# Kernel optimization log

Measured on AMD Instinct MI355X. Metric: run time of the kernel, lower is better.

The kernel has to match this reference:

```python
import jax, jax.numpy as jnp
import numpy as np


def _butter1(Wn, highpass):
    """First-order Butterworth digital coefficients (bilinear transform),
    matching scipy.signal.butter(1, Wn, btype). Wn is nyquist-normalized."""
    K = jnp.tan(jnp.pi * Wn / 2.0)
    a1 = (K - 1.0) / (K + 1.0)
    if highpass:
        b0 = 1.0 / (K + 1.0)
        b1 = -b0
    else:
        b0 = K / (K + 1.0)
        b1 = b0
    return b0, b1, a1


def setup_inputs() -> dict:
    key = jax.random.key(0)
    B, T = 128, 262144
    x = jax.random.normal(key, (B, T), dtype=jnp.float32)
    return {
        "x": x,
        "center_freq": jnp.float32(1000.0),  # nn.Parameter
        "bandwidth": jnp.float32(500.0),     # nn.Parameter
        "gain": jnp.float32(1.0),            # nn.Parameter
        "sample_rate": 48000,
    }


def reference(x, center_freq, bandwidth, gain, sample_rate):
    nyq = sample_rate / 2.0
    low_wn = (center_freq - bandwidth / 2.0) / nyq
    high_wn = (center_freq + bandwidth / 2.0) / nyq
    # cascaded 1st-order highpass(low_wn) then lowpass(high_wn) = bandpass
    bh0, bh1, ah1 = _butter1(low_wn, highpass=True)
    bl0, bl1, al1 = _butter1(high_wn, highpass=False)

    xt = x.T  # [T, B] -- scan over time, vectorized over batch
    zeros = jnp.zeros((x.shape[0],), dtype=x.dtype)

    def step(carry, x_t):
        x_prev, y1_prev, y2_prev = carry
        y1 = bh0 * x_t + bh1 * x_prev - ah1 * y1_prev   # highpass stage
        y2 = bl0 * y1 + bl1 * y1_prev - al1 * y2_prev   # lowpass stage
        return (x_t, y1, y2), y2

    _, yt = jax.lax.scan(step, (zeros, zeros, zeros), xt)
    return yt.T * gain  # [B, T]
```

## Files before the change

### kernel.cpp

```cpp
#include <hip/hip_runtime.h>
#include <math.h>

#define B_    128
#define T_    262144
#define L_    16
#define NT_   256
#define WCH_  16
#define OT_   (NT_ * L_)
#define TPR_  (T_ / OT_)
#define NW_   (NT_ / 64)
#define STR_  (L_ + 1)
#define GPB_  4
#define NBLK_ ((B_ * TPR_) / GPB_)

typedef float f32x4 __attribute__((ext_vector_type(4)));

struct Coef {
    float bh0, bh1;
    float p, q, r;
    float blc0, blc1;
};

__device__ inline void iir_step(const Coef& c, float xt, float& x_prev,
                                float& y1, float& y2) {
    float c1 = fmaf(c.bh0,  xt, c.bh1  * x_prev);
    float cx = fmaf(c.blc0, xt, c.blc1 * x_prev);
    float ny1 = fmaf(c.p, y1, c1);
    float ny2 = fmaf(c.q, y1, fmaf(c.r, y2, cx));
    y1 = ny1; y2 = ny2; x_prev = xt;
}

struct Mat { float p, q, r; };
__device__ inline Mat mat_sq(Mat m) {
    Mat o; o.p = m.p * m.p; o.q = m.q * (m.p + m.r); o.r = m.r * m.r; return o;
}
__device__ inline Mat mat_mul(Mat a, Mat b) {
    Mat o; o.p = a.p * b.p; o.q = fmaf(a.q, b.p, a.r * b.q); o.r = a.r * b.r;
    return o;
}
__device__ inline float2 mat_apply_add(Mat m, float2 v, float2 add) {
    float2 o;
    o.x = fmaf(m.p, v.x, add.x);
    o.y = fmaf(m.q, v.x, fmaf(m.r, v.y, add.y));
    return o;
}

__global__ __launch_bounds__(NT_, 4) void bp_kernel(
        const float* __restrict__ x, float* __restrict__ out,
        const float* __restrict__ cfp, const float* __restrict__ bwp,
        const float* __restrict__ gp, const int* __restrict__ srp) {
    __shared__ float  ys[NT_ * STR_];
    __shared__ float2 wagg[WCH_];
    __shared__ float2 wsagg[NW_];

    const int blk  = blockIdx.x;
    const int t    = threadIdx.x;
    const int lane = t & 63;
    const int wav  = t >> 6;

    const int tid0 = blk * GPB_;
    const int row  = tid0 >> 6;
    const int ti0  = tid0 & (TPR_ - 1);
    const long base0 = (long)row * T_ + (long)ti0 * OT_;

    {
        const float* xb = x + base0;
        (void)xb;
    }
    const float* xb0 = x + base0;
    const f32x4* xg0 = (const f32x4*)(xb0 + t * L_);
    f32x4 v0 = __builtin_nontemporal_load(xg0 + 0);
    f32x4 v1 = __builtin_nontemporal_load(xg0 + 1);
    f32x4 v2 = __builtin_nontemporal_load(xg0 + 2);
    f32x4 v3 = __builtin_nontemporal_load(xg0 + 3);
    f32x4 w0 = (f32x4)(0.f), w1 = w0, w2 = w0, w3 = w0;
    if (t < WCH_ && ti0 != 0) {
        const f32x4* wg = (const f32x4*)(xb0 - WCH_ * L_ + t * L_);
        w0 = wg[0]; w1 = wg[1]; w2 = wg[2]; w3 = wg[3];
    }
    float lxp = 0.f;
    if (lane == 0 && (ti0 != 0 || t != 0)) lxp = xb0[t * L_ - 1];

    Coef cf;
    {
        const float PIH = 1.57079632679489661923f;
        float cfv = *cfp, bwv = *bwp;
        float nyq = 0.5f * (float)(*srp);
        float K1 = tanf(PIH * (cfv - 0.5f * bwv) / nyq);
        float K2 = tanf(PIH * (cfv + 0.5f * bwv) / nyq);
        float inv1 = 1.0f / (K1 + 1.0f);
        float ah1 = (K1 - 1.0f) * inv1;
        float inv2 = 1.0f / (K2 + 1.0f);
        float bl0 = K2 * inv2;
        float al1 = (K2 - 1.0f) * inv2;
        cf.bh0 = inv1;
        cf.bh1 = -inv1;
        cf.p = -ah1;
        cf.q = bl0 - bl0 * ah1;
        cf.r = -al1;
        cf.blc0 = bl0 * inv1;
        cf.blc1 = -bl0 * inv1;
    }
    const float gain = *gp;

    Mat A  = { cf.p, cf.q, cf.r };
    Mat AL = A;
    #pragma unroll
    for (int k = 0; k < 4; ++k) AL = mat_sq(AL);
    Mat R = { 1.f, 0.f, 1.f };
    {
        Mat Mp = AL;
        unsigned b = (unsigned)lane;
        #pragma unroll
        for (int k = 0; k < 6; ++k) {
            if (b & 1u) R = mat_mul(Mp, R);
            b >>= 1u;
            if (k < 5) Mp = mat_sq(Mp);
        }
    }

    float2 Scar = make_float2(0.f, 0.f);

    #pragma unroll
    for (int g = 0; g < GPB_; ++g) {
        const long base = base0 + (long)g * OT_;

        float xp = __shfl_up(v3.w, 1u, 64);
        if (lane == 0) xp = lxp;

        float xa[L_];
        xa[0]=v0.x; xa[1]=v0.y; xa[2]=v0.z; xa[3]=v0.w;
        xa[4]=v1.x; xa[5]=v1.y; xa[6]=v1.z; xa[7]=v1.w;
        xa[8]=v2.x; xa[9]=v2.y; xa[10]=v2.z; xa[11]=v2.w;
        xa[12]=v3.x; xa[13]=v3.y; xa[14]=v3.z; xa[15]=v3.w;
        float y2l[L_];
        float y1 = 0.f, y2 = 0.f;
        {
            float xprev = xp;
            #pragma unroll
            for (int i = 0; i < L_; ++i) {
                iir_step(cf, xa[i], xprev, y1, y2);
                y2l[i] = y2;
            }
        }

        if (g == 0) {
            float wxp = __shfl_up(w3.w, 1u, 64);
            if (t < WCH_) {
                float wa[L_];
                wa[0]=w0.x; wa[1]=w0.y; wa[2]=w0.z; wa[3]=w0.w;
                wa[4]=w1.x; wa[5]=w1.y; wa[6]=w1.z; wa[7]=w1.w;
                wa[8]=w2.x; wa[9]=w2.y; wa[10]=w2.z; wa[11]=w2.w;
                wa[12]=w3.x; wa[13]=w3.y; wa[14]=w3.z; wa[15]=w3.w;
                float wy1 = 0.f, wy2 = 0.f;
                float wp = (t == 0) ? 0.f : wxp;
                #pragma unroll
                for (int i = 0; i < L_; ++i) iir_step(cf, wa[i], wp, wy1, wy2);
                wagg[t] = make_float2(wy1, wy2);
            }
        }

        if (g + 1 < GPB_) {
            const float* nxb = x + base + OT_;
            const f32x4* nxg = (const f32x4*)(nxb + t * L_);
            v0 = __builtin_nontemporal_load(nxg + 0);
            v1 = __builtin_nontemporal_load(nxg + 1);
            v2 = __builtin_nontemporal_load(nxg + 2);
            v3 = __builtin_nontemporal_load(nxg + 3);
            if (lane == 0) lxp = nxb[t * L_ - 1];
        }

        float2 a = make_float2(y1, y2);
        Mat Pw = AL;
        #pragma unroll
        for (int o = 1; o < 64; o <<= 1) {
            float vx = __shfl_up(a.x, (unsigned)o, 64);
            float vy = __shfl_up(a.y, (unsigned)o, 64);
            if (lane >= o) {
                a.y = fmaf(Pw.q, vx, fmaf(Pw.r, vy, a.y));
                a.x = fmaf(Pw.p, vx, a.x);
            }
            Pw = mat_sq(Pw);
        }
        float2 ex;
        ex.x = __shfl_up(a.x, 1u, 64);
        ex.y = __shfl_up(a.y, 1u, 64);
        if (lane == 0) { ex.x = 0.f; ex.y = 0.f; }
        if (lane == 63) wsagg[wav] = a;
        __syncthreads();

        float2 S;
        if (g == 0) {
            S = make_float2(0.f, 0.f);
            #pragma unroll
            for (int j = 0; j < WCH_; ++j) S = mat_apply_add(AL, S, wagg[j]);
        } else {
            S = Scar;
        }

        {
            float2 Stot = wsagg[0];
            #pragma unroll
            for (int u = 1; u < NW_; ++u) Stot = mat_apply_add(Pw, Stot, wsagg[u]);
            Mat P2 = mat_sq(Pw);
            Mat P4 = mat_sq(P2);
            Scar = mat_apply_add(P4, S, Stot);
        }

        float2 Sw = S;
        #pragma unroll
        for (int u = 0; u < NW_ - 1; ++u)
            if (wav > u) Sw = mat_apply_add(Pw, Sw, wsagg[u]);
        float2 E = mat_apply_add(R, Sw, ex);

        {
            float c1 = E.x, c2 = E.y;
            float* cp = ys + t * STR_;
            #pragma unroll
            for (int i = 0; i < L_; ++i) {
                float nc1 = cf.p * c1;
                float nc2 = fmaf(cf.q, c1, cf.r * c2);
                c1 = nc1; c2 = nc2;
                cp[i] = (y2l[i] + c2) * gain;
            }
        }
        __syncthreads();

        f32x4* og = (f32x4*)(out + base);
        #pragma unroll
        for (int k = 0; k < 4; ++k) {
            int F = t + NT_ * k;
            int chunk = F >> 2, pos = 4 * (F & 3);
            const float* p = ys + chunk * STR_ + pos;
            f32x4 o; o.x = p[0]; o.y = p[1]; o.z = p[2]; o.w = p[3];
            __builtin_nontemporal_store(o, og + F);
        }
    }
}

extern "C" void kernel_launch(void* const* d_in, const int* in_sizes, int n_in,
                              void* d_out, int out_size, void* d_ws, size_t ws_size,
                              hipStream_t stream) {
    const float* x   = (const float*)d_in[0];
    const float* cfp = (const float*)d_in[1];
    const float* bwp = (const float*)d_in[2];
    const float* gp  = (const float*)d_in[3];
    const int*   srp = (const int*)d_in[4];
    float* out = (float*)d_out;

    dim3 blk(NT_), grd(NBLK_);
    bp_kernel<<<grd, blk, 0, stream>>>(x, out, cfp, bwp, gp, srp);
}
```

Measured before the change: 243.1 us.

## Recompute IIR from carry and store directly, dropping LDS transpose staging

The output pass no longer keeps 16 partial outputs and transposes them through shared memory. Each thread instead reruns the IIR over its 16 inputs starting from the exact carry state and writes four float4 values straight to global memory. This removes one __syncthreads and the LDS round trip per group, and the wave-sum buffer is double-buffered so the next group does not overwrite it early. Groups per block grow from 4 to 8 and the group loop is no longer unrolled. The cost is that each thread now writes a 64-byte span of its own, which is less coalesced than the old transposed stores, and the recurrence arithmetic is doubled.

```diff
diff --git a/kernel.cpp b/kernel.cpp
--- a/kernel.cpp
+++ b/kernel.cpp
@@ -9,8 +9,7 @@
 #define OT_   (NT_ * L_)
 #define TPR_  (T_ / OT_)
 #define NW_   (NT_ / 64)
-#define STR_  (L_ + 1)
-#define GPB_  4
+#define GPB_  8
 #define NBLK_ ((B_ * TPR_) / GPB_)
 
 typedef float f32x4 __attribute__((ext_vector_type(4)));
@@ -49,9 +48,8 @@
         const float* __restrict__ x, float* __restrict__ out,
         const float* __restrict__ cfp, const float* __restrict__ bwp,
         const float* __restrict__ gp, const int* __restrict__ srp) {
-    __shared__ float  ys[NT_ * STR_];
     __shared__ float2 wagg[WCH_];
-    __shared__ float2 wsagg[NW_];
+    __shared__ float2 wsagg[2][NW_];
 
     const int blk  = blockIdx.x;
     const int t    = threadIdx.x;
@@ -63,10 +61,6 @@
     const int ti0  = tid0 & (TPR_ - 1);
     const long base0 = (long)row * T_ + (long)ti0 * OT_;
 
-    {
-        const float* xb = x + base0;
-        (void)xb;
-    }
     const float* xb0 = x + base0;
     const f32x4* xg0 = (const f32x4*)(xb0 + t * L_);
     f32x4 v0 = __builtin_nontemporal_load(xg0 + 0);
@@ -119,55 +113,54 @@
         }
     }
 
+    {
+        float wxp = __shfl_up(w3.w, 1u, 64);
+        if (t < WCH_) {
+            float wy1 = 0.f, wy2 = 0.f;
+            float wp = (t == 0) ? 0.f : wxp;
+            iir_step(cf, w0.x, wp, wy1, wy2); iir_step(cf, w0.y, wp, wy1, wy2);
+            iir_step(cf, w0.z, wp, wy1, wy2); iir_step(cf, w0.w, wp, wy1, wy2);
+            iir_step(cf, w1.x, wp, wy1, wy2); iir_step(cf, w1.y, wp, wy1, wy2);
+            iir_step(cf, w1.z, wp, wy1, wy2); iir_step(cf, w1.w, wp, wy1, wy2);
+            iir_step(cf, w2.x, wp, wy1, wy2); iir_step(cf, w2.y, wp, wy1, wy2);
+            iir_step(cf, w2.z, wp, wy1, wy2); iir_step(cf, w2.w, wp, wy1, wy2);
+            iir_step(cf, w3.x, wp, wy1, wy2); iir_step(cf, w3.y, wp, wy1, wy2);
+            iir_step(cf, w3.z, wp, wy1, wy2); iir_step(cf, w3.w, wp, wy1, wy2);
+            wagg[t] = make_float2(wy1, wy2);
+        }
+    }
+
     float2 Scar = make_float2(0.f, 0.f);
 
-    #pragma unroll
     for (int g = 0; g < GPB_; ++g) {
         const long base = base0 + (long)g * OT_;
 
         float xp = __shfl_up(v3.w, 1u, 64);
         if (lane == 0) xp = lxp;
 
-        float xa[L_];
-        xa[0]=v0.x; xa[1]=v0.y; xa[2]=v0.z; xa[3]=v0.w;
-        xa[4]=v1.x; xa[5]=v1.y; xa[6]=v1.z; xa[7]=v1.w;
-        xa[8]=v2.x; xa[9]=v2.y; xa[10]=v2.z; xa[11]=v2.w;
-        xa[12]=v3.x; xa[13]=v3.y; xa[14]=v3.z; xa[15]=v3.w;
-        float y2l[L_];
         float y1 = 0.f, y2 = 0.f;
         {
             float xprev = xp;
-            #pragma unroll
-            for (int i = 0; i < L_; ++i) {
-                iir_step(cf, xa[i], xprev, y1, y2);
-                y2l[i] = y2;
-            }
-        }
-
-        if (g == 0) {
-            float wxp = __shfl_up(w3.w, 1u, 64);
-            if (t < WCH_) {
-                float wa[L_];
-                wa[0]=w0.x; wa[1]=w0.y; wa[2]=w0.z; wa[3]=w0.w;
-                wa[4]=w1.x; wa[5]=w1.y; wa[6]=w1.z; wa[7]=w1.w;
-                wa[8]=w2.x; wa[9]=w2.y; wa[10]=w2.z; wa[11]=w2.w;
-                wa[12]=w3.x; wa[13]=w3.y; wa[14]=w3.z; wa[15]=w3.w;
-                float wy1 = 0.f, wy2 = 0.f;
-                float wp = (t == 0) ? 0.f : wxp;
-                #pragma unroll
-                for (int i = 0; i < L_; ++i) iir_step(cf, wa[i], wp, wy1, wy2);
-                wagg[t] = make_float2(wy1, wy2);
-            }
-        }
-
+            iir_step(cf, v0.x, xprev, y1, y2); iir_step(cf, v0.y, xprev, y1, y2);
+            iir_step(cf, v0.z, xprev, y1, y2); iir_step(cf, v0.w, xprev, y1, y2);
+            iir_step(cf, v1.x, xprev, y1, y2); iir_step(cf, v1.y, xprev, y1, y2);
+            iir_step(cf, v1.z, xprev, y1, y2); iir_step(cf, v1.w, xprev, y1, y2);
+            iir_step(cf, v2.x, xprev, y1, y2); iir_step(cf, v2.y, xprev, y1, y2);
+            iir_step(cf, v2.z, xprev, y1, y2); iir_step(cf, v2.w, xprev, y1, y2);
+            iir_step(cf, v3.x, xprev, y1, y2); iir_step(cf, v3.y, xprev, y1, y2);
+            iir_step(cf, v3.z, xprev, y1, y2); iir_step(cf, v3.w, xprev, y1, y2);
+        }
+
+        f32x4 p0, p1, p2, p3;
+        float plxp = 0.f;
         if (g + 1 < GPB_) {
             const float* nxb = x + base + OT_;
             const f32x4* nxg = (const f32x4*)(nxb + t * L_);
-            v0 = __builtin_nontemporal_load(nxg + 0);
-            v1 = __builtin_nontemporal_load(nxg + 1);
-            v2 = __builtin_nontemporal_load(nxg + 2);
-            v3 = __builtin_nontemporal_load(nxg + 3);
-            if (lane == 0) lxp = nxb[t * L_ - 1];
+            p0 = __builtin_nontemporal_load(nxg + 0);
+            p1 = __builtin_nontemporal_load(nxg + 1);
+            p2 = __builtin_nontemporal_load(nxg + 2);
+            p3 = __builtin_nontemporal_load(nxg + 3);
+            if (lane == 0) plxp = nxb[t * L_ - 1];
         }
 
         float2 a = make_float2(y1, y2);
@@ -186,7 +179,8 @@
         ex.x = __shfl_up(a.x, 1u, 64);
         ex.y = __shfl_up(a.y, 1u, 64);
         if (lane == 0) { ex.x = 0.f; ex.y = 0.f; }
-        if (lane == 63) wsagg[wav] = a;
+        float2* wsb = wsagg[g & 1];
+        if (lane == 63) wsb[wav] = a;
         __syncthreads();
 
         float2 S;
@@ -199,9 +193,9 @@
         }
 
         {
-            float2 Stot = wsagg[0];
+            float2 Stot = wsb[0];
             #pragma unroll
-            for (int u = 1; u < NW_; ++u) Stot = mat_apply_add(Pw, Stot, wsagg[u]);
+            for (int u = 1; u < NW_; ++u) Stot = mat_apply_add(Pw, Stot, wsb[u]);
             Mat P2 = mat_sq(Pw);
             Mat P4 = mat_sq(P2);
             Scar = mat_apply_add(P4, S, Stot);
@@ -210,30 +204,38 @@
         float2 Sw = S;
         #pragma unroll
         for (int u = 0; u < NW_ - 1; ++u)
-            if (wav > u) Sw = mat_apply_add(Pw, Sw, wsagg[u]);
+            if (wav > u) Sw = mat_apply_add(Pw, Sw, wsb[u]);
         float2 E = mat_apply_add(R, Sw, ex);
 
         {
-            float c1 = E.x, c2 = E.y;
-            float* cp = ys + t * STR_;
-            #pragma unroll
-            for (int i = 0; i < L_; ++i) {
-                float nc1 = cf.p * c1;
-                float nc2 = fmaf(cf.q, c1, cf.r * c2);
-                c1 = nc1; c2 = nc2;
-                cp[i] = (y2l[i] + c2) * gain;
-            }
-        }
-        __syncthreads();
-
-        f32x4* og = (f32x4*)(out + base);
-        #pragma unroll
-        for (int k = 0; k < 4; ++k) {
-            int F = t + NT_ * k;
-            int chunk = F >> 2, pos = 4 * (F & 3);
-            const float* p = ys + chunk * STR_ + pos;
-            f32x4 o; o.x = p[0]; o.y = p[1]; o.z = p[2]; o.w = p[3];
-            __builtin_nontemporal_store(o, og + F);
+            f32x4* og = (f32x4*)(out + base + (long)t * L_);
+            float ty1 = E.x, ty2 = E.y, xprev = xp;
+            f32x4 o;
+            iir_step(cf, v0.x, xprev, ty1, ty2); o.x = ty2 * gain;
+            iir_step(cf, v0.y, xprev, ty1, ty2); o.y = ty2 * gain;
+            iir_step(cf, v0.z, xprev, ty1, ty2); o.z = ty2 * gain;
+            iir_step(cf, v0.w, xprev, ty1, ty2); o.w = ty2 * gain;
+            og[0] = o;
+            iir_step(cf, v1.x, xprev, ty1, ty2); o.x = ty2 * gain;
+            iir_step(cf, v1.y, xprev, ty1, ty2); o.y = ty2 * gain;
+            iir_step(cf, v1.z, xprev, ty1, ty2); o.z = ty2 * gain;
+            iir_step(cf, v1.w, xprev, ty1, ty2); o.w = ty2 * gain;
+            og[1] = o;
+            iir_step(cf, v2.x, xprev, ty1, ty2); o.x = ty2 * gain;
+            iir_step(cf, v2.y, xprev, ty1, ty2); o.y = ty2 * gain;
+            iir_step(cf, v2.z, xprev, ty1, ty2); o.z = ty2 * gain;
+            iir_step(cf, v2.w, xprev, ty1, ty2); o.w = ty2 * gain;
+            og[2] = o;
+            iir_step(cf, v3.x, xprev, ty1, ty2); o.x = ty2 * gain;
+            iir_step(cf, v3.y, xprev, ty1, ty2); o.y = ty2 * gain;
+            iir_step(cf, v3.z, xprev, ty1, ty2); o.z = ty2 * gain;
+            iir_step(cf, v3.w, xprev, ty1, ty2); o.w = ty2 * gain;
+            og[3] = o;
+        }
+
+        if (g + 1 < GPB_) {
+            v0 = p0; v1 = p1; v2 = p2; v3 = p3;
+            lxp = plxp;
         }
     }
 }
```

After: 260.0 us. 7.0% more time.
